# Kernel optimization log

Measured on AMD Instinct MI355X. Metric: run time of the kernel, lower is better.

Reference implementation:

```python
import jax, jax.numpy as jnp
import numpy as np

B = 100        # number of queries
N = 50000      # n_node
E = 600000     # n_edges
D = 128        # in_dim = out_dim (hidden_dim)
A = 64         # attn_dim
R = 200        # n_rel -> rela_embed has 2*R+1 = 401 rows


def setup_inputs() -> dict:
    key = jax.random.key(0)
    ks = jax.random.split(key, 14)
    q_sub = jax.random.randint(ks[0], (B,), 0, N)
    q_rel = jax.random.randint(ks[1], (B,), 0, 2 * R + 1)
    # edges: [E, 6]; col0=r_idx(<B), col2=rel(<2R+1), col4=sub(<N), col5=obj(<N); cols 1,3 unused
    c0 = jax.random.randint(ks[2], (E,), 0, B)
    c2 = jax.random.randint(ks[3], (E,), 0, 2 * R + 1)
    c4 = jax.random.randint(ks[4], (E,), 0, N)
    c5 = jax.random.randint(ks[5], (E,), 0, N)
    z = jnp.zeros((E,), dtype=jnp.int32)
    edges = jnp.stack([c0, z, c2, z, c4, c5], axis=1)
    hidden = jax.random.normal(ks[6], (N, D), dtype=jnp.float32)
    # learned parameters
    rela_embed = jax.random.normal(ks[7], (2 * R + 1, D), dtype=jnp.float32) * 0.02
    Ws = jax.random.normal(ks[8], (D, A), dtype=jnp.float32) * 0.05   # Ws_attn.weight^T
    Wr = jax.random.normal(ks[9], (D, A), dtype=jnp.float32) * 0.05   # Wr_attn.weight^T
    Wqr = jax.random.normal(ks[10], (D, A), dtype=jnp.float32) * 0.05 # Wqr_attn.weight^T
    bqr = jnp.zeros((A,), dtype=jnp.float32)
    wa = jax.random.normal(ks[11], (A, 1), dtype=jnp.float32) * 0.05  # w_alpha.weight^T
    ba = jnp.zeros((1,), dtype=jnp.float32)
    Wh = jax.random.normal(ks[12], (D, D), dtype=jnp.float32) * 0.05  # W_h.weight^T
    return {"q_sub": q_sub, "q_rel": q_rel, "hidden": hidden, "edges": edges,
            "n_node": N, "rela_embed": rela_embed, "Ws": Ws, "Wr": Wr,
            "Wqr": Wqr, "bqr": bqr, "wa": wa, "ba": ba, "Wh": Wh}


def reference(q_sub, q_rel, hidden, edges, n_node, rela_embed, Ws, Wr, Wqr, bqr, wa, ba, Wh):
    sub = edges[:, 4]
    rel = edges[:, 2]
    obj = edges[:, 5]
    r_idx = edges[:, 0]
    hs = hidden[sub]                       # [E, D] gather
    hr = rela_embed[rel]                   # [E, D] gather
    h_qr = rela_embed[q_rel][r_idx]        # [B, D] then gather -> [E, D]
    # attention score per edge
    pre = hs @ Ws + hr @ Wr + h_qr @ Wqr + bqr          # [E, A]
    alpha = jax.nn.sigmoid(jax.nn.relu(pre) @ wa + ba)   # [E, 1]
    message = alpha * (hs + hr)                          # [E, D]
    message_agg = jax.ops.segment_sum(message, obj, num_segments=n_node)  # [N, D]
    hidden_new = message_agg @ Wh                        # act = identity ('idd')
    return hidden_new
```

## Files before the change

kernel.cpp:

```cpp
#include <hip/hip_runtime.h>

#define DD 128
#define AA 64
#define SS 160

static inline int idiv_up(int a, int b) { return (a + b - 1) / b; }

__device__ __forceinline__ unsigned short f2bf(float f) {
    unsigned u = __float_as_uint(f);
    u += 0x7fff + ((u >> 16) & 1);
    return (unsigned short)(u >> 16);
}
__device__ __forceinline__ float bf2f(unsigned short h) {
    return __uint_as_float(((unsigned)h) << 16);
}

__global__ __launch_bounds__(256)
void proj_hist_kernel(const float* __restrict__ hidden,
                      const float* __restrict__ rela,
                      const int* __restrict__ q_rel,
                      const float* __restrict__ Ws,
                      const float* __restrict__ Wr,
                      const float* __restrict__ Wqr,
                      const float* __restrict__ bqr,
                      const float* __restrict__ Wh,
                      const int* __restrict__ edges,
                      int* __restrict__ deg,
                      float* __restrict__ subrows,
                      float* __restrict__ hrWr,
                      float* __restrict__ relaWh,
                      float* __restrict__ hqrWqr,
                      int N, int NR, int B, int E,
                      int nA, int nB, int nC, int nH) {
    __shared__ float lht[128 * 64];
    __shared__ float wbuf[128 * 64];
    const int t = threadIdx.x;
    const int bid = blockIdx.x;

    if (bid & 1) {
        const int hb = bid >> 1;
        if (hb >= nH) return;
        const int ebase = hb * 1024;
        #pragma unroll
        for (int j = 0; j < 4; ++j) {
            const int e = ebase + j * 256 + t;
            if (e < E) atomicAdd(&deg[edges[(long)e * 6 + 5]], 1);
        }
        return;
    }

    const int pb = bid >> 1;
    if (pb >= nA + nB + nC) return;
    int type, rbase, nrows;
    const float* src;
    if (pb < nA)           { type = 0; rbase = pb * 64;             nrows = N;  src = hidden; }
    else if (pb < nA + nB) { type = 1; rbase = (pb - nA) * 64;      nrows = NR; src = rela; }
    else                   { type = 2; rbase = (pb - nA - nB) * 64; nrows = B;  src = rela; }

    const int row = t & 63;
    const int d0 = (t >> 6) * 32;
    const int gr = rbase + row;
    const float* srow = nullptr;
    if (gr < nrows) {
        const int sr = (type == 2) ? q_rel[gr] : gr;
        srow = src + (long)sr * DD;
    }
    #pragma unroll
    for (int j = 0; j < 8; ++j) {
        float4 v = make_float4(0.f, 0.f, 0.f, 0.f);
        if (srow) v = *(const float4*)&srow[d0 + j * 4];
        lht[(d0 + j * 4 + 0) * 64 + row] = v.x;
        lht[(d0 + j * 4 + 1) * 64 + row] = v.y;
        lht[(d0 + j * 4 + 2) * 64 + row] = v.z;
        lht[(d0 + j * 4 + 3) * 64 + row] = v.w;
    }

    const int r0 = (t & 15) * 4;
    const int c0 = (t >> 4) * 4;
    const int nph = (type == 2) ? 1 : 3;

    for (int p = 0; p < nph; ++p) {
        const float* W;
        int ldw, off;
        if (p == 0) {
            W = (type == 0) ? Ws : (type == 1) ? Wr : Wqr;
            ldw = 64; off = 0;
        } else {
            W = Wh; ldw = 128; off = (p - 1) * 64;
        }
        #pragma unroll
        for (int k = 0; k < 8192; k += 1024) {
            const int f = k + t * 4;
            *(float4*)&wbuf[f] = *(const float4*)&W[(long)(f >> 6) * ldw + off + (f & 63)];
        }
        __syncthreads();

        float acc[4][4] = {};
        #pragma unroll 4
        for (int d = 0; d < 128; ++d) {
            const float4 hv = *(const float4*)&lht[d * 64 + r0];
            const float4 wv = *(const float4*)&wbuf[d * 64 + c0];
            acc[0][0] = fmaf(hv.x, wv.x, acc[0][0]);
            acc[0][1] = fmaf(hv.x, wv.y, acc[0][1]);
            acc[0][2] = fmaf(hv.x, wv.z, acc[0][2]);
            acc[0][3] = fmaf(hv.x, wv.w, acc[0][3]);
            acc[1][0] = fmaf(hv.y, wv.x, acc[1][0]);
            acc[1][1] = fmaf(hv.y, wv.y, acc[1][1]);
            acc[1][2] = fmaf(hv.y, wv.z, acc[1][2]);
            acc[1][3] = fmaf(hv.y, wv.w, acc[1][3]);
            acc[2][0] = fmaf(hv.z, wv.x, acc[2][0]);
            acc[2][1] = fmaf(hv.z, wv.y, acc[2][1]);
            acc[2][2] = fmaf(hv.z, wv.z, acc[2][2]);
            acc[2][3] = fmaf(hv.z, wv.w, acc[2][3]);
            acc[3][0] = fmaf(hv.w, wv.x, acc[3][0]);
            acc[3][1] = fmaf(hv.w, wv.y, acc[3][1]);
            acc[3][2] = fmaf(hv.w, wv.z, acc[3][2]);
            acc[3][3] = fmaf(hv.w, wv.w, acc[3][3]);
        }

        #pragma unroll
        for (int i = 0; i < 4; ++i) {
            const int orow = rbase + r0 + i;
            if (orow >= nrows) continue;
            if (type == 0) {
                float* srw = subrows + (long)orow * SS;
                if (p == 0) {
                    ushort4 o;
                    o.x = f2bf(acc[i][0]); o.y = f2bf(acc[i][1]);
                    o.z = f2bf(acc[i][2]); o.w = f2bf(acc[i][3]);
                    *(ushort4*)((unsigned short*)srw + c0) = o;
                } else {
                    *(float4*)(srw + 32 + off + c0) =
                        make_float4(acc[i][0], acc[i][1], acc[i][2], acc[i][3]);
                }
            } else if (type == 1) {
                if (p == 0) {
                    *(float4*)&hrWr[(long)orow * 64 + c0] =
                        make_float4(acc[i][0], acc[i][1], acc[i][2], acc[i][3]);
                } else {
                    *(float4*)&relaWh[(long)orow * 128 + off + c0] =
                        make_float4(acc[i][0], acc[i][1], acc[i][2], acc[i][3]);
                }
            } else {
                const float4 bq = *(const float4*)&bqr[c0];
                *(float4*)&hqrWqr[(long)orow * 64 + c0] =
                    make_float4(acc[i][0] + bq.x, acc[i][1] + bq.y,
                                acc[i][2] + bq.z, acc[i][3] + bq.w);
            }
        }
        __syncthreads();
    }
}

__global__ __launch_bounds__(1024)
void scan_kernel(const int* __restrict__ deg, int* __restrict__ offs,
                 int* __restrict__ cur, int N) {
    __shared__ int wsum[17];
    const int t = threadIdx.x;
    const int lane = t & 63;
    const int wv = t >> 6;
    int carry = 0;
    for (int base = 0; base < N; base += 4096) {
        const int i0 = base + t * 4;
        int v0 = 0, v1 = 0, v2 = 0, v3 = 0;
        if (i0 + 3 < N) {
            const int4 q = *(const int4*)&deg[i0];
            v0 = q.x; v1 = q.y; v2 = q.z; v3 = q.w;
        } else {
            if (i0 + 0 < N) v0 = deg[i0 + 0];
            if (i0 + 1 < N) v1 = deg[i0 + 1];
            if (i0 + 2 < N) v2 = deg[i0 + 2];
            if (i0 + 3 < N) v3 = deg[i0 + 3];
        }
        const int s = v0 + v1 + v2 + v3;
        int inc = s;
        #pragma unroll
        for (int o = 1; o < 64; o <<= 1) {
            const int x = __shfl_up(inc, o, 64);
            if (lane >= o) inc += x;
        }
        if (lane == 63) wsum[wv] = inc;
        __syncthreads();
        if (t == 0) {
            int run = 0;
            #pragma unroll
            for (int k = 0; k < 16; ++k) { const int tmp = wsum[k]; wsum[k] = run; run += tmp; }
            wsum[16] = run;
        }
        __syncthreads();
        int e = carry + wsum[wv] + (inc - s);
        if (i0 + 0 < N) { offs[i0 + 0] = e; cur[i0 + 0] = e; } e += v0;
        if (i0 + 1 < N) { offs[i0 + 1] = e; cur[i0 + 1] = e; } e += v1;
        if (i0 + 2 < N) { offs[i0 + 2] = e; cur[i0 + 2] = e; } e += v2;
        if (i0 + 3 < N) { offs[i0 + 3] = e; cur[i0 + 3] = e; } e += v3;
        carry += wsum[16];
        __syncthreads();
    }
}

__global__ void scatter_kernel(const int* __restrict__ edges, int* cur,
                               int2* __restrict__ recs, int E) {
    const int e = blockIdx.x * blockDim.x + threadIdx.x;
    if (e >= E) return;
    const int2 a = *(const int2*)&edges[(long)e * 6];
    const int2 b = *(const int2*)&edges[(long)e * 6 + 2];
    const int2 c = *(const int2*)&edges[(long)e * 6 + 4];
    const int pos = atomicAdd(&cur[c.y], 1);
    recs[pos] = make_int2(c.x, b.x | (a.x << 16));
}

__global__ __launch_bounds__(256)
void gather_kernel(const int2* __restrict__ recs,
                   const int* __restrict__ offs,
                   const float* __restrict__ subrows,
                   const float* __restrict__ hrWr,
                   const float* __restrict__ hqrWqr,
                   const float* __restrict__ relaWh,
                   const float* __restrict__ wa,
                   const float* __restrict__ ba,
                   float* __restrict__ out, int N, int E) {
    const int lane = threadIdx.x & 63;
    const int g = lane >> 4;
    const int l = lane & 15;
    const int v = (int)((blockIdx.x * blockDim.x + threadIdx.x) >> 6);
    if (v >= N) return;
    const float4 wav = *(const float4*)&wa[l * 4];
    const float bar = ba[0];
    const int start = offs[v];
    const int end = (v + 1 < N) ? offs[v + 1] : E;

    float4 acc0 = make_float4(0.f, 0.f, 0.f, 0.f);
    float4 acc1 = make_float4(0.f, 0.f, 0.f, 0.f);

    for (int base = start; base < end; base += 8) {
        const int k1 = base + g;
        const int k2 = base + 4 + g;
        const bool va1 = (k1 < end);
        const bool va2 = (k2 < end);
        const int2 rc1 = va1 ? recs[k1] : make_int2(0, 0);
        const int2 rc2 = va2 ? recs[k2] : make_int2(0, 0);
        const int sub1 = rc1.x, rel1 = rc1.y & 0xffff, rid1 = rc1.y >> 16;
        const int sub2 = rc2.x, rel2 = rc2.y & 0xffff, rid2 = rc2.y >> 16;
        const float* sr1 = subrows + (long)sub1 * SS;
        const float* sr2 = subrows + (long)sub2 * SS;

        const ushort4 hw1 = *(const ushort4*)((const unsigned short*)sr1 + l * 4);
        const ushort4 hw2 = *(const ushort4*)((const unsigned short*)sr2 + l * 4);
        const float4 b41 = *(const float4*)&hrWr[rel1 * AA + l * 4];
        const float4 b42 = *(const float4*)&hrWr[rel2 * AA + l * 4];
        const float4 c41 = *(const float4*)&hqrWqr[rid1 * AA + l * 4];
        const float4 c42 = *(const float4*)&hqrWqr[rid2 * AA + l * 4];
        const float4 h01 = *(const float4*)(sr1 + 32 + l * 8);
        const float4 h11 = *(const float4*)(sr1 + 32 + l * 8 + 4);
        const float4 h02 = *(const float4*)(sr2 + 32 + l * 8);
        const float4 h12 = *(const float4*)(sr2 + 32 + l * 8 + 4);
        const float4 r01 = *(const float4*)&relaWh[rel1 * DD + l * 8];
        const float4 r11 = *(const float4*)&relaWh[rel1 * DD + l * 8 + 4];
        const float4 r02 = *(const float4*)&relaWh[rel2 * DD + l * 8];
        const float4 r12 = *(const float4*)&relaWh[rel2 * DD + l * 8 + 4];

        float s1 = fmaxf(bf2f(hw1.x) + b41.x + c41.x, 0.f) * wav.x;
        s1 = fmaf(fmaxf(bf2f(hw1.y) + b41.y + c41.y, 0.f), wav.y, s1);
        s1 = fmaf(fmaxf(bf2f(hw1.z) + b41.z + c41.z, 0.f), wav.z, s1);
        s1 = fmaf(fmaxf(bf2f(hw1.w) + b41.w + c41.w, 0.f), wav.w, s1);
        float s2 = fmaxf(bf2f(hw2.x) + b42.x + c42.x, 0.f) * wav.x;
        s2 = fmaf(fmaxf(bf2f(hw2.y) + b42.y + c42.y, 0.f), wav.y, s2);
        s2 = fmaf(fmaxf(bf2f(hw2.z) + b42.z + c42.z, 0.f), wav.z, s2);
        s2 = fmaf(fmaxf(bf2f(hw2.w) + b42.w + c42.w, 0.f), wav.w, s2);
        s1 += __shfl_xor(s1, 1);  s2 += __shfl_xor(s2, 1);
        s1 += __shfl_xor(s1, 2);  s2 += __shfl_xor(s2, 2);
        s1 += __shfl_xor(s1, 4);  s2 += __shfl_xor(s2, 4);
        s1 += __shfl_xor(s1, 8);  s2 += __shfl_xor(s2, 8);
        float al1 = __builtin_amdgcn_rcpf(1.0f + __expf(-(s1 + bar)));
        float al2 = __builtin_amdgcn_rcpf(1.0f + __expf(-(s2 + bar)));
        if (!va1) al1 = 0.0f;
        if (!va2) al2 = 0.0f;

        acc0.x = fmaf(al1, h01.x + r01.x, acc0.x);
        acc0.y = fmaf(al1, h01.y + r01.y, acc0.y);
        acc0.z = fmaf(al1, h01.z + r01.z, acc0.z);
        acc0.w = fmaf(al1, h01.w + r01.w, acc0.w);
        acc1.x = fmaf(al1, h11.x + r11.x, acc1.x);
        acc1.y = fmaf(al1, h11.y + r11.y, acc1.y);
        acc1.z = fmaf(al1, h11.z + r11.z, acc1.z);
        acc1.w = fmaf(al1, h11.w + r11.w, acc1.w);
        acc0.x = fmaf(al2, h02.x + r02.x, acc0.x);
        acc0.y = fmaf(al2, h02.y + r02.y, acc0.y);
        acc0.z = fmaf(al2, h02.z + r02.z, acc0.z);
        acc0.w = fmaf(al2, h02.w + r02.w, acc0.w);
        acc1.x = fmaf(al2, h12.x + r12.x, acc1.x);
        acc1.y = fmaf(al2, h12.y + r12.y, acc1.y);
        acc1.z = fmaf(al2, h12.z + r12.z, acc1.z);
        acc1.w = fmaf(al2, h12.w + r12.w, acc1.w);
    }

    #pragma unroll
    for (int o = 16; o <= 32; o <<= 1) {
        acc0.x += __shfl_xor(acc0.x, o);
        acc0.y += __shfl_xor(acc0.y, o);
        acc0.z += __shfl_xor(acc0.z, o);
        acc0.w += __shfl_xor(acc0.w, o);
        acc1.x += __shfl_xor(acc1.x, o);
        acc1.y += __shfl_xor(acc1.y, o);
        acc1.z += __shfl_xor(acc1.z, o);
        acc1.w += __shfl_xor(acc1.w, o);
    }
    if (g == 0) {
        *(float4*)&out[(long)v * DD + l * 8]     = acc0;
        *(float4*)&out[(long)v * DD + l * 8 + 4] = acc1;
    }
}

extern "C" void kernel_launch(void* const* d_in, const int* in_sizes, int n_in,
                              void* d_out, int out_size, void* d_ws, size_t ws_size,
                              hipStream_t stream) {
    const int*   q_rel  = (const int*)d_in[1];
    const float* hidden = (const float*)d_in[2];
    const int*   edges  = (const int*)d_in[3];
    const float* rela   = (const float*)d_in[5];
    const float* Ws     = (const float*)d_in[6];
    const float* Wr     = (const float*)d_in[7];
    const float* Wqr    = (const float*)d_in[8];
    const float* bqr    = (const float*)d_in[9];
    const float* wa     = (const float*)d_in[10];
    const float* ba     = (const float*)d_in[11];
    const float* Wh     = (const float*)d_in[12];

    const int B  = in_sizes[1];
    const int N  = in_sizes[2] / DD;
    const int E  = in_sizes[3] / 6;
    const int NR = in_sizes[5] / DD;

    float* out = (float*)d_out;

    float* subrows = (float*)d_ws;
    float* hrWr    = subrows + (size_t)N * SS;
    float* relaWh  = hrWr + (size_t)NR * AA;
    float* hqrWqr  = relaWh + (size_t)NR * DD;
    int*   deg     = (int*)(hqrWqr + (size_t)B * AA);
    int*   cur     = deg  + N;
    int*   offs    = cur  + N;
    int2*  recs    = (int2*)(offs + N);

    const int nA = idiv_up(N, 64);
    const int nB = idiv_up(NR, 64);
    const int nC = idiv_up(B, 64);
    const int nH = idiv_up(E, 1024);
    const int nP = nA + nB + nC;
    const int grid_ph = 2 * ((nP > nH) ? nP : nH);

    hipMemsetAsync(deg, 0, (size_t)N * sizeof(int), stream);
    proj_hist_kernel<<<grid_ph, 256, 0, stream>>>(
        hidden, rela, q_rel, Ws, Wr, Wqr, bqr, Wh, edges, deg,
        subrows, hrWr, relaWh, hqrWqr, N, NR, B, E, nA, nB, nC, nH);
    scan_kernel<<<1, 1024, 0, stream>>>(deg, offs, cur, N);
    scatter_kernel<<<idiv_up(E, 256), 256, 0, stream>>>(edges, cur, recs, E);
    gather_kernel<<<idiv_up(N * 64, 256), 256, 0, stream>>>(
        recs, offs, subrows, hrWr, hqrWqr, relaWh, wa, ba, out, N, E);
}
```

Before: 320.5 us.

## Store hidden@Wh projections in bf16, split histogram kernel, use multi-block scan

Stores the per-node hidden@Wh rows in bf16 instead of fp32, shrinking each subrow from 160 to 96 float-equivalents and cutting gather traffic. The histogram is moved out of the projection kernel into its own kernel. The projection kernel now reads the weights directly from global memory instead of staging them in shared memory. The single-block scan is replaced by a multi-block scan that uses a last-block-done fixup, so offsets become a local offset plus a per-block base. The bf16 messages reduce precision, the weight reads lose shared-memory reuse, and the extra launch adds overhead.

```diff
diff --git a/kernel.cpp b/kernel.cpp
--- a/kernel.cpp
+++ b/kernel.cpp
@@ -2,7 +2,7 @@
 
 #define DD 128
 #define AA 64
-#define SS 160
+#define SS 96
 
 static inline int idiv_up(int a, int b) { return (a + b - 1) / b; }
 
@@ -16,46 +16,27 @@
 }
 
 __global__ __launch_bounds__(256)
-void proj_hist_kernel(const float* __restrict__ hidden,
-                      const float* __restrict__ rela,
-                      const int* __restrict__ q_rel,
-                      const float* __restrict__ Ws,
-                      const float* __restrict__ Wr,
-                      const float* __restrict__ Wqr,
-                      const float* __restrict__ bqr,
-                      const float* __restrict__ Wh,
-                      const int* __restrict__ edges,
-                      int* __restrict__ deg,
-                      float* __restrict__ subrows,
-                      float* __restrict__ hrWr,
-                      float* __restrict__ relaWh,
-                      float* __restrict__ hqrWqr,
-                      int N, int NR, int B, int E,
-                      int nA, int nB, int nC, int nH) {
+void proj_all_kernel(const float* __restrict__ hidden,
+                     const float* __restrict__ rela,
+                     const int* __restrict__ q_rel,
+                     const float* __restrict__ Ws,
+                     const float* __restrict__ Wr,
+                     const float* __restrict__ Wqr,
+                     const float* __restrict__ bqr,
+                     const float* __restrict__ Wh,
+                     float* __restrict__ subrows,
+                     float* __restrict__ hrWr,
+                     float* __restrict__ relaWh,
+                     float* __restrict__ hqrWqr,
+                     int N, int NR, int B, int nA, int nB) {
     __shared__ float lht[128 * 64];
-    __shared__ float wbuf[128 * 64];
     const int t = threadIdx.x;
     const int bid = blockIdx.x;
-
-    if (bid & 1) {
-        const int hb = bid >> 1;
-        if (hb >= nH) return;
-        const int ebase = hb * 1024;
-        #pragma unroll
-        for (int j = 0; j < 4; ++j) {
-            const int e = ebase + j * 256 + t;
-            if (e < E) atomicAdd(&deg[edges[(long)e * 6 + 5]], 1);
-        }
-        return;
-    }
-
-    const int pb = bid >> 1;
-    if (pb >= nA + nB + nC) return;
     int type, rbase, nrows;
     const float* src;
-    if (pb < nA)           { type = 0; rbase = pb * 64;             nrows = N;  src = hidden; }
-    else if (pb < nA + nB) { type = 1; rbase = (pb - nA) * 64;      nrows = NR; src = rela; }
-    else                   { type = 2; rbase = (pb - nA - nB) * 64; nrows = B;  src = rela; }
+    if (bid < nA)           { type = 0; rbase = bid * 64;             nrows = N;  src = hidden; }
+    else if (bid < nA + nB) { type = 1; rbase = (bid - nA) * 64;      nrows = NR; src = rela; }
+    else                    { type = 2; rbase = (bid - nA - nB) * 64; nrows = B;  src = rela; }
 
     const int row = t & 63;
     const int d0 = (t >> 6) * 32;
@@ -74,6 +55,7 @@
         lht[(d0 + j * 4 + 2) * 64 + row] = v.z;
         lht[(d0 + j * 4 + 3) * 64 + row] = v.w;
     }
+    __syncthreads();
 
     const int r0 = (t & 15) * 4;
     const int c0 = (t >> 4) * 4;
@@ -88,18 +70,13 @@
         } else {
             W = Wh; ldw = 128; off = (p - 1) * 64;
         }
-        #pragma unroll
-        for (int k = 0; k < 8192; k += 1024) {
-            const int f = k + t * 4;
-            *(float4*)&wbuf[f] = *(const float4*)&W[(long)(f >> 6) * ldw + off + (f & 63)];
-        }
-        __syncthreads();
+        const float* wp = W + off + c0;
 
         float acc[4][4] = {};
         #pragma unroll 4
         for (int d = 0; d < 128; ++d) {
             const float4 hv = *(const float4*)&lht[d * 64 + r0];
-            const float4 wv = *(const float4*)&wbuf[d * 64 + c0];
+            const float4 wv = *(const float4*)&wp[(long)d * ldw];
             acc[0][0] = fmaf(hv.x, wv.x, acc[0][0]);
             acc[0][1] = fmaf(hv.x, wv.y, acc[0][1]);
             acc[0][2] = fmaf(hv.x, wv.z, acc[0][2]);
@@ -124,14 +101,13 @@
             if (orow >= nrows) continue;
             if (type == 0) {
                 float* srw = subrows + (long)orow * SS;
+                ushort4 o;
+                o.x = f2bf(acc[i][0]); o.y = f2bf(acc[i][1]);
+                o.z = f2bf(acc[i][2]); o.w = f2bf(acc[i][3]);
                 if (p == 0) {
-                    ushort4 o;
-                    o.x = f2bf(acc[i][0]); o.y = f2bf(acc[i][1]);
-                    o.z = f2bf(acc[i][2]); o.w = f2bf(acc[i][3]);
                     *(ushort4*)((unsigned short*)srw + c0) = o;
                 } else {
-                    *(float4*)(srw + 32 + off + c0) =
-                        make_float4(acc[i][0], acc[i][1], acc[i][2], acc[i][3]);
+                    *(ushort4*)((unsigned short*)(srw + 32) + off + c0) = o;
                 }
             } else if (type == 1) {
                 if (p == 0) {
@@ -148,70 +124,81 @@
                                 acc[i][2] + bq.z, acc[i][3] + bq.w);
             }
         }
+    }
+}
+
+__global__ void hist_kernel(const int* __restrict__ edges, int* deg, int E) {
+    const int e = blockIdx.x * blockDim.x + threadIdx.x;
+    if (e < E) atomicAdd(&deg[edges[(long)e * 6 + 5]], 1);
+}
+
+__global__ __launch_bounds__(256)
+void scan_kernel(const int* __restrict__ deg, int* __restrict__ loff,
+                 int* __restrict__ cur, int* __restrict__ bsum,
+                 int* __restrict__ bsumx, int* __restrict__ done,
+                 int n, int nb) {
+    __shared__ int tsum[256];
+    __shared__ int lastFlag;
+    const int t = threadIdx.x;
+    const int b = blockIdx.x;
+    const int base = b * 1024 + t * 4;
+    int v[4];
+    int s = 0;
+    #pragma unroll
+    for (int j = 0; j < 4; ++j) {
+        v[j] = (base + j < n) ? deg[base + j] : 0;
+        s += v[j];
+    }
+    tsum[t] = s;
+    __syncthreads();
+    for (int o = 1; o < 256; o <<= 1) {
+        const int x = (t >= o) ? tsum[t - o] : 0;
         __syncthreads();
-    }
-}
-
-__global__ __launch_bounds__(1024)
-void scan_kernel(const int* __restrict__ deg, int* __restrict__ offs,
-                 int* __restrict__ cur, int N) {
-    __shared__ int wsum[17];
-    const int t = threadIdx.x;
-    const int lane = t & 63;
-    const int wv = t >> 6;
-    int carry = 0;
-    for (int base = 0; base < N; base += 4096) {
-        const int i0 = base + t * 4;
-        int v0 = 0, v1 = 0, v2 = 0, v3 = 0;
-        if (i0 + 3 < N) {
-            const int4 q = *(const int4*)&deg[i0];
-            v0 = q.x; v1 = q.y; v2 = q.z; v3 = q.w;
-        } else {
-            if (i0 + 0 < N) v0 = deg[i0 + 0];
-            if (i0 + 1 < N) v1 = deg[i0 + 1];
-            if (i0 + 2 < N) v2 = deg[i0 + 2];
-            if (i0 + 3 < N) v3 = deg[i0 + 3];
-        }
-        const int s = v0 + v1 + v2 + v3;
-        int inc = s;
+        tsum[t] += x;
+        __syncthreads();
+    }
+    int run = (t > 0) ? tsum[t - 1] : 0;
+    #pragma unroll
+    for (int j = 0; j < 4; ++j) {
+        if (base + j < n) { loff[base + j] = run; cur[base + j] = run; }
+        run += v[j];
+    }
+    if (t == 255) {
+        bsum[b] = tsum[255];
+        __threadfence();
+    }
+    __syncthreads();
+    if (t == 0) lastFlag = (atomicAdd(done, 1) == nb - 1);
+    __syncthreads();
+    if (lastFlag && t < 64) {
+        __threadfence();
+        const int val = (t < nb) ? bsum[t] : 0;
+        int inc = val;
         #pragma unroll
         for (int o = 1; o < 64; o <<= 1) {
             const int x = __shfl_up(inc, o, 64);
-            if (lane >= o) inc += x;
+            if (t >= o) inc += x;
         }
-        if (lane == 63) wsum[wv] = inc;
-        __syncthreads();
-        if (t == 0) {
-            int run = 0;
-            #pragma unroll
-            for (int k = 0; k < 16; ++k) { const int tmp = wsum[k]; wsum[k] = run; run += tmp; }
-            wsum[16] = run;
-        }
-        __syncthreads();
-        int e = carry + wsum[wv] + (inc - s);
-        if (i0 + 0 < N) { offs[i0 + 0] = e; cur[i0 + 0] = e; } e += v0;
-        if (i0 + 1 < N) { offs[i0 + 1] = e; cur[i0 + 1] = e; } e += v1;
-        if (i0 + 2 < N) { offs[i0 + 2] = e; cur[i0 + 2] = e; } e += v2;
-        if (i0 + 3 < N) { offs[i0 + 3] = e; cur[i0 + 3] = e; } e += v3;
-        carry += wsum[16];
-        __syncthreads();
+        if (t < nb) bsumx[t] = inc - val;
     }
 }
 
 __global__ void scatter_kernel(const int* __restrict__ edges, int* cur,
+                               const int* __restrict__ bsumx,
                                int2* __restrict__ recs, int E) {
     const int e = blockIdx.x * blockDim.x + threadIdx.x;
     if (e >= E) return;
     const int2 a = *(const int2*)&edges[(long)e * 6];
     const int2 b = *(const int2*)&edges[(long)e * 6 + 2];
     const int2 c = *(const int2*)&edges[(long)e * 6 + 4];
-    const int pos = atomicAdd(&cur[c.y], 1);
+    const int pos = bsumx[c.y >> 10] + atomicAdd(&cur[c.y], 1);
     recs[pos] = make_int2(c.x, b.x | (a.x << 16));
 }
 
 __global__ __launch_bounds__(256)
 void gather_kernel(const int2* __restrict__ recs,
-                   const int* __restrict__ offs,
+                   const int* __restrict__ loff,
+                   const int* __restrict__ bsumx,
                    const float* __restrict__ subrows,
                    const float* __restrict__ hrWr,
                    const float* __restrict__ hqrWqr,
@@ -226,8 +213,8 @@
     if (v >= N) return;
     const float4 wav = *(const float4*)&wa[l * 4];
     const float bar = ba[0];
-    const int start = offs[v];
-    const int end = (v + 1 < N) ? offs[v + 1] : E;
+    const int start = loff[v] + bsumx[v >> 10];
+    const int end = (v + 1 < N) ? (loff[v + 1] + bsumx[(v + 1) >> 10]) : E;
 
     float4 acc0 = make_float4(0.f, 0.f, 0.f, 0.f);
     float4 acc1 = make_float4(0.f, 0.f, 0.f, 0.f);
@@ -250,10 +237,10 @@
         const float4 b42 = *(const float4*)&hrWr[rel2 * AA + l * 4];
         const float4 c41 = *(const float4*)&hqrWqr[rid1 * AA + l * 4];
         const float4 c42 = *(const float4*)&hqrWqr[rid2 * AA + l * 4];
-        const float4 h01 = *(const float4*)(sr1 + 32 + l * 8);
-        const float4 h11 = *(const float4*)(sr1 + 32 + l * 8 + 4);
-        const float4 h02 = *(const float4*)(sr2 + 32 + l * 8);
-        const float4 h12 = *(const float4*)(sr2 + 32 + l * 8 + 4);
+        const ushort4 m01 = *(const ushort4*)((const unsigned short*)(sr1 + 32) + l * 8);
+        const ushort4 m11 = *(const ushort4*)((const unsigned short*)(sr1 + 32) + l * 8 + 4);
+        const ushort4 m02 = *(const ushort4*)((const unsigned short*)(sr2 + 32) + l * 8);
+        const ushort4 m12 = *(const ushort4*)((const unsigned short*)(sr2 + 32) + l * 8 + 4);
         const float4 r01 = *(const float4*)&relaWh[rel1 * DD + l * 8];
         const float4 r11 = *(const float4*)&relaWh[rel1 * DD + l * 8 + 4];
         const float4 r02 = *(const float4*)&relaWh[rel2 * DD + l * 8];
@@ -276,22 +263,22 @@
         if (!va1) al1 = 0.0f;
         if (!va2) al2 = 0.0f;
 
-        acc0.x = fmaf(al1, h01.x + r01.x, acc0.x);
-        acc0.y = fmaf(al1, h01.y + r01.y, acc0.y);
-        acc0.z = fmaf(al1, h01.z + r01.z, acc0.z);
-        acc0.w = fmaf(al1, h01.w + r01.w, acc0.w);
-        acc1.x = fmaf(al1, h11.x + r11.x, acc1.x);
-        acc1.y = fmaf(al1, h11.y + r11.y, acc1.y);
-        acc1.z = fmaf(al1, h11.z + r11.z, acc1.z);
-        acc1.w = fmaf(al1, h11.w + r11.w, acc1.w);
-        acc0.x = fmaf(al2, h02.x + r02.x, acc0.x);
-        acc0.y = fmaf(al2, h02.y + r02.y, acc0.y);
-        acc0.z = fmaf(al2, h02.z + r02.z, acc0.z);
-        acc0.w = fmaf(al2, h02.w + r02.w, acc0.w);
-        acc1.x = fmaf(al2, h12.x + r12.x, acc1.x);
-        acc1.y = fmaf(al2, h12.y + r12.y, acc1.y);
-        acc1.z = fmaf(al2, h12.z + r12.z, acc1.z);
-        acc1.w = fmaf(al2, h12.w + r12.w, acc1.w);
+        acc0.x = fmaf(al1, bf2f(m01.x) + r01.x, acc0.x);
+        acc0.y = fmaf(al1, bf2f(m01.y) + r01.y, acc0.y);
+        acc0.z = fmaf(al1, bf2f(m01.z) + r01.z, acc0.z);
+        acc0.w = fmaf(al1, bf2f(m01.w) + r01.w, acc0.w);
+        acc1.x = fmaf(al1, bf2f(m11.x) + r11.x, acc1.x);
+        acc1.y = fmaf(al1, bf2f(m11.y) + r11.y, acc1.y);
+        acc1.z = fmaf(al1, bf2f(m11.z) + r11.z, acc1.z);
+        acc1.w = fmaf(al1, bf2f(m11.w) + r11.w, acc1.w);
+        acc0.x = fmaf(al2, bf2f(m02.x) + r02.x, acc0.x);
+        acc0.y = fmaf(al2, bf2f(m02.y) + r02.y, acc0.y);
+        acc0.z = fmaf(al2, bf2f(m02.z) + r02.z, acc0.z);
+        acc0.w = fmaf(al2, bf2f(m02.w) + r02.w, acc0.w);
+        acc1.x = fmaf(al2, bf2f(m12.x) + r12.x, acc1.x);
+        acc1.y = fmaf(al2, bf2f(m12.y) + r12.y, acc1.y);
+        acc1.z = fmaf(al2, bf2f(m12.z) + r12.z, acc1.z);
+        acc1.w = fmaf(al2, bf2f(m12.w) + r12.w, acc1.w);
     }
 
     #pragma unroll
@@ -338,23 +325,25 @@
     float* relaWh  = hrWr + (size_t)NR * AA;
     float* hqrWqr  = relaWh + (size_t)NR * DD;
     int*   deg     = (int*)(hqrWqr + (size_t)B * AA);
-    int*   cur     = deg  + N;
-    int*   offs    = cur  + N;
-    int2*  recs    = (int2*)(offs + N);
+    int*   done    = deg + N;
+    int*   cur     = done + 3;
+    int*   loff    = cur + N;
+    int*   bsum    = loff + N;
+    int*   bsumx   = bsum + 64;
+    int2*  recs    = (int2*)(bsumx + 64);
 
     const int nA = idiv_up(N, 64);
     const int nB = idiv_up(NR, 64);
     const int nC = idiv_up(B, 64);
-    const int nH = idiv_up(E, 1024);
-    const int nP = nA + nB + nC;
-    const int grid_ph = 2 * ((nP > nH) ? nP : nH);
-
-    hipMemsetAsync(deg, 0, (size_t)N * sizeof(int), stream);
-    proj_hist_kernel<<<grid_ph, 256, 0, stream>>>(
-        hidden, rela, q_rel, Ws, Wr, Wqr, bqr, Wh, edges, deg,
-        subrows, hrWr, relaWh, hqrWqr, N, NR, B, E, nA, nB, nC, nH);
-    scan_kernel<<<1, 1024, 0, stream>>>(deg, offs, cur, N);
-    scatter_kernel<<<idiv_up(E, 256), 256, 0, stream>>>(edges, cur, recs, E);
+    const int nb = idiv_up(N, 1024);
+
+    hipMemsetAsync(deg, 0, (size_t)(N + 1) * sizeof(int), stream);
+    proj_all_kernel<<<nA + nB + nC, 256, 0, stream>>>(
+        hidden, rela, q_rel, Ws, Wr, Wqr, bqr, Wh,
+        subrows, hrWr, relaWh, hqrWqr, N, NR, B, nA, nB);
+    hist_kernel<<<idiv_up(E, 256), 256, 0, stream>>>(edges, deg, E);
+    scan_kernel<<<nb, 256, 0, stream>>>(deg, loff, cur, bsum, bsumx, done, N, nb);
+    scatter_kernel<<<idiv_up(E, 256), 256, 0, stream>>>(edges, cur, bsumx, recs, E);
     gather_kernel<<<idiv_up(N * 64, 256), 256, 0, stream>>>(
-        recs, offs, subrows, hrWr, hqrWqr, relaWh, wa, ba, out, N, E);
-}
+        recs, loff, bsumx, subrows, hrWr, hqrWqr, relaWh, wa, ba, out, N, E);
+}
```

New measurement: 289.5 us. -9.7%, faster.
